# Optimization experiments

Measured on AMD Instinct MI355X. Metric: run time of the kernel, lower is better.

The kernel has to match this reference:

```python
import jax, jax.numpy as jnp
import numpy as np

N, C_IN, C_OUT, P, W, H = 32, 32, 16, 4, 16, 16
D = P * P
EPS = 1e-6


def squash(s, axis=-1):
    # v = ||s||^2/(1+||s||^2) * s/||s||, eps-stabilized as in the repo (eps=1e-6)
    n2 = jnp.sum(s * s, axis=axis, keepdims=True)
    n = jnp.sqrt(n2)
    return (n2 / (1.0 + n2)) * s / (n + EPS)


def setup_inputs() -> dict:
    key = jax.random.key(0)
    k1, k2, k3 = jax.random.split(key, 3)
    l = jax.random.normal(k1, (N, C_IN, D, W, H), jnp.float32)
    g = jax.random.normal(k2, (N, C_OUT, D), jnp.float32)
    weight = jax.random.normal(k3, (1, C_IN, 1, C_OUT, P, P), jnp.float32)
    return {"l": l, "g": g, "weight": weight, "num_iters": 3}


def reference(l, g, weight, num_iters):
    n, c, d, w, h = l.shape
    p = weight.shape[-1]
    c_out = weight.shape[3]
    # (N, C, D, W, H) -> (N, C, W*H, P, P)
    lp = jnp.transpose(l, (0, 1, 3, 4, 2)).reshape(n, c, w * h, p, p)
    # votes: pose matmul against per-(in,out) transform matrices
    # v[n,c,s,o] = lp[n,c,s] @ weight[0,c,0,o]   -> (N, C, WH, C_out, P, P)
    v = jnp.einsum('ncsij,cojk->ncsoik', lp, weight[0, :, 0])
    M = c * w * h
    v = v.reshape(n, M, c_out, d)          # (N, M, C_out, D)
    g = g[:, None, :, :]                    # (N, 1, C_out, D)
    # dynamic routing, logits initialized from agreement with the prior global capsule g
    b = jnp.sum(v * g, axis=-1, keepdims=True)   # (N, M, C_out, 1)
    cc = None
    for _ in range(num_iters):
        cc = jax.nn.softmax(b, axis=1)           # attention over input votes M
        g = squash(jnp.sum(cc * v, axis=1, keepdims=True))  # (N, 1, C_out, D)
        b = b + jnp.sum(v * g, axis=-1, keepdims=True)
    a = jnp.squeeze(cc, -1)   # (N, M, C_out)
    g = jnp.squeeze(g, 1)     # (N, C_out, D)
    return a, g
```

## Files before the change

kernel.cpp:

```cpp
#include <hip/hip_runtime.h>
#include <math.h>

#define N_   32
#define CIN  32
#define COUT 16
#define D_   16
#define S_   256
#define M_   (CIN * S_)

#define LOG2E 1.4426950408889634f

#define PROW 20
#define PIDX(n, c, o) ((((size_t)(n) * CIN + (c)) * COUT + (o)) * PROW)

#define WS_PB0 0
#define WS_PB1 (N_ * CIN * COUT * PROW)
#define WS_G1  (2 * N_ * CIN * COUT * PROW)

#define SW(s) ((((s) & 3)) ^ (((s) >> 2) & 3))

__device__ __forceinline__ void stage_tile(const float* __restrict__ gsrc,
                                           float* ls, int tid) {
  const float4* src = (const float4*)gsrc;
#pragma unroll
  for (int j = 0; j < 4; j++) {
    int f = ((tid & 3) << 6) + (tid >> 2) + (j << 8);
    float4 val = src[f];
    int dd = f >> 6;
    int u  = f & 63;
    int chunk = dd >> 2, lo = dd & 3;
    float vv[4] = {val.x, val.y, val.z, val.w};
#pragma unroll
    for (int m = 0; m < 4; m++) {
      int s = (u << 2) + m;
      int p = chunk ^ SW(s);
      ls[(s << 4) + (p << 2) + lo] = vv[m];
    }
  }
}

__device__ __forceinline__ void read_lp(const float* ls, int s, float* lp) {
  const float4* row = (const float4*)(ls + (s << 4));
  int sw = SW(s);
#pragma unroll
  for (int c = 0; c < 4; c++) {
    float4 q = row[c ^ sw];
    lp[c * 4 + 0] = q.x; lp[c * 4 + 1] = q.y;
    lp[c * 4 + 2] = q.z; lp[c * 4 + 3] = q.w;
  }
}

__device__ __forceinline__ float dot16(const float* a, const float* b) {
  float a0 = 0.f, a1 = 0.f, a2 = 0.f, a3 = 0.f;
#pragma unroll
  for (int k = 0; k < 4; k++) {
    a0 = fmaf(a[k],      b[k],      a0);
    a1 = fmaf(a[4 + k],  b[4 + k],  a1);
    a2 = fmaf(a[8 + k],  b[8 + k],  a2);
    a3 = fmaf(a[12 + k], b[12 + k], a3);
  }
  return (a0 + a1) + (a2 + a3);
}

__global__ __launch_bounds__(256, 3) void pass_kernel(
    const float* __restrict__ l, const float* __restrict__ wgt,
    const float* __restrict__ gprev, const float* __restrict__ part_in,
    float* __restrict__ gstore, float* __restrict__ part_out,
    float* __restrict__ edump, int mode) {
  const int bid = blockIdx.x;
  const int n = bid >> 5;
  const int c = bid & 31;
  const int tid = threadIdx.x;
  const int o = tid & 15;
  const int strip = tid >> 4;

  __shared__ float ls[D_ * S_];
  __shared__ float red[4][18][16];
  __shared__ float red2[18][16];
  __shared__ float hd[16][20];

  if (mode && tid < 64) {
    const int ho = tid & 15, hs = tid >> 4;
    float H[18];
#pragma unroll
    for (int f = 0; f < 17; f++) H[f] = 0.f;
    H[17] = -INFINITY;
#pragma unroll 2
    for (int q = 0; q < 8; q++) {
      const float* r = part_in + PIDX(n, hs + 4 * q, ho);
      const float4* r4 = (const float4*)r;
#pragma unroll
      for (int i = 0; i < 4; i++) {
        float4 v = r4[i];
        H[i * 4 + 0] += v.x; H[i * 4 + 1] += v.y;
        H[i * 4 + 2] += v.z; H[i * 4 + 3] += v.w;
      }
      H[16] += r[16];
      H[17] = fmaxf(H[17], r[17]);
    }
#pragma unroll
    for (int off = 16; off <= 32; off <<= 1) {
#pragma unroll
      for (int f = 0; f < 17; f++) H[f] += __shfl_xor(H[f], off);
      H[17] = fmaxf(H[17], __shfl_xor(H[17], off));
    }
    if (tid < 16) {
      float inv = 1.0f / H[16], n2 = 0.f, Sg[16];
#pragma unroll
      for (int d = 0; d < 16; d++) { Sg[d] = H[d] * inv; n2 = fmaf(Sg[d], Sg[d], n2); }
      float coef = n2 / ((1.f + n2) * (sqrtf(n2) + 1e-6f));
      float4* hq = (float4*)hd[tid];
#pragma unroll
      for (int i = 0; i < 4; i++)
        hq[i] = make_float4(coef * Sg[i * 4 + 0], coef * Sg[i * 4 + 1],
                            coef * Sg[i * 4 + 2], coef * Sg[i * 4 + 3]);
      hd[tid][16] = H[17];
    }
  }

  stage_tile(l + ((size_t)(n * CIN + c)) * D_ * S_, ls, tid);

  float Greg[16];
  {
    const float4* gp = (const float4*)(gprev + (n * COUT + o) * 16);
#pragma unroll
    for (int i = 0; i < 4; i++) {
      float4 u = gp[i];
      Greg[i * 4 + 0] = u.x; Greg[i * 4 + 1] = u.y;
      Greg[i * 4 + 2] = u.z; Greg[i * 4 + 3] = u.w;
    }
  }

  __syncthreads();

  float shift = 0.f;
  if (mode) {
    const float4* hq = (const float4*)hd[o];
#pragma unroll
    for (int i = 0; i < 4; i++) {
      float4 v = hq[i];
      Greg[i * 4 + 0] += v.x; Greg[i * 4 + 1] += v.y;
      Greg[i * 4 + 2] += v.z; Greg[i * 4 + 3] += v.w;
    }
    shift = hd[o][16];
    if (mode == 1 && c == 0 && tid < 16) {
      float* gs = gstore + (n * COUT + tid) * 16;
      const float4* hp = (const float4*)hd[tid];
      const float4* gp = (const float4*)(gprev + (n * COUT + tid) * 16);
      float4* g4 = (float4*)gs;
#pragma unroll
      for (int i = 0; i < 4; i++) {
        float4 a = gp[i], b = hp[i];
        g4[i] = make_float4(a.x + b.x, a.y + b.y, a.z + b.z, a.w + b.w);
      }
    }
  }

  float WG[16];
  {
    float wreg[16];
    const float4* wp = (const float4*)(wgt + (c * COUT + o) * 16);
#pragma unroll
    for (int i = 0; i < 4; i++) {
      float4 t = wp[i];
      wreg[i * 4 + 0] = t.x; wreg[i * 4 + 1] = t.y;
      wreg[i * 4 + 2] = t.z; wreg[i * 4 + 3] = t.w;
    }
#pragma unroll
    for (int i = 0; i < 4; i++)
#pragma unroll
      for (int j = 0; j < 4; j++) {
        float acc = 0.f;
#pragma unroll
        for (int k = 0; k < 4; k++)
          acc = fmaf(wreg[j * 4 + k], Greg[i * 4 + k], acc);
        WG[i * 4 + j] = acc * LOG2E;
      }
  }

  float se = 0.f, bmx = -INFINITY, E[16];
#pragma unroll
  for (int d = 0; d < 16; d++) E[d] = 0.f;

#pragma unroll 4
  for (int it = 0; it < 16; it++) {
    float lp[16];
    read_lp(ls, strip + (it << 4), lp);
    float b = dot16(lp, WG) - shift;
    float e = exp2f(b);
    if (mode == 2) {
      edump[((size_t)(n * M_ + c * S_ + strip + (it << 4))) * COUT + o] = e;
    }
    bmx = fmaxf(bmx, b);
    se += e;
#pragma unroll
    for (int d = 0; d < 16; d++) E[d] = fmaf(e, lp[d], E[d]);
  }

#pragma unroll
  for (int off = 16; off <= 32; off <<= 1) {
    se += __shfl_xor(se, off);
    bmx = fmaxf(bmx, __shfl_xor(bmx, off));
#pragma unroll
    for (int d = 0; d < 16; d++) E[d] += __shfl_xor(E[d], off);
  }

  const int w = tid >> 6;
  if ((tid & 63) < 16) {
#pragma unroll
    for (int d = 0; d < 16; d++) red[w][d][o] = E[d];
    red[w][16][o] = se;
    red[w][17][o] = bmx;
  }
  __syncthreads();

  for (int p = tid; p < 288; p += 256) {
    int f = p >> 4, oo = p & 15;
    float v0 = red[0][f][oo], v1 = red[1][f][oo];
    float v2 = red[2][f][oo], v3 = red[3][f][oo];
    red2[f][oo] = (f == 17) ? fmaxf(fmaxf(v0, v1), fmaxf(v2, v3))
                            : ((v0 + v1) + (v2 + v3));
  }
  __syncthreads();

  if (tid < 16) {
    float wt[16];
    const float4* wp = (const float4*)(wgt + (c * COUT + tid) * 16);
#pragma unroll
    for (int i = 0; i < 4; i++) {
      float4 t = wp[i];
      wt[i * 4 + 0] = t.x; wt[i * 4 + 1] = t.y;
      wt[i * 4 + 2] = t.z; wt[i * 4 + 3] = t.w;
    }
    float Et[16];
#pragma unroll
    for (int d = 0; d < 16; d++) Et[d] = red2[d][tid];
    float* p0 = part_out + PIDX(n, c, tid);
    float4* p4 = (float4*)p0;
#pragma unroll
    for (int i = 0; i < 4; i++) {
      float s0 = 0.f, s1 = 0.f, s2 = 0.f, s3 = 0.f;
#pragma unroll
      for (int j = 0; j < 4; j++) {
        s0 = fmaf(Et[i * 4 + j], wt[j * 4 + 0], s0);
        s1 = fmaf(Et[i * 4 + j], wt[j * 4 + 1], s1);
        s2 = fmaf(Et[i * 4 + j], wt[j * 4 + 2], s2);
        s3 = fmaf(Et[i * 4 + j], wt[j * 4 + 3], s3);
      }
      p4[i] = make_float4(s0, s1, s2, s3);
    }
    p0[16] = red2[16][tid];
    p0[17] = red2[17][tid] + shift;
  }
}

__global__ __launch_bounds__(256, 4) void a_kernel(
    const float* __restrict__ part, float* __restrict__ a_out,
    float* __restrict__ g_out) {
  const int bid = blockIdx.x;
  const int n = bid >> 6;
  const int chunk = bid & 63;
  const int tid = threadIdx.x;

  __shared__ float sinv[16];

  if (tid < 16) {
    float se = 0.f;
    if (chunk == 0) {
      float S[16];
#pragma unroll
      for (int d = 0; d < 16; d++) S[d] = 0.f;
#pragma unroll 4
      for (int c = 0; c < CIN; c++) {
        const float* r = part + PIDX(n, c, tid);
        const float4* r4 = (const float4*)r;
#pragma unroll
        for (int i = 0; i < 4; i++) {
          float4 v = r4[i];
          S[i * 4 + 0] += v.x; S[i * 4 + 1] += v.y;
          S[i * 4 + 2] += v.z; S[i * 4 + 3] += v.w;
        }
        se += r[16];
      }
      float inv = 1.0f / se, n2 = 0.f;
#pragma unroll
      for (int d = 0; d < 16; d++) { S[d] *= inv; n2 = fmaf(S[d], S[d], n2); }
      float coef = n2 / ((1.f + n2) * (sqrtf(n2) + 1e-6f));
      float* go = g_out + (n * COUT + tid) * 16;
#pragma unroll
      for (int d = 0; d < 16; d++) go[d] = coef * S[d];
      sinv[tid] = inv;
    } else {
#pragma unroll 8
      for (int c = 0; c < CIN; c++) se += part[PIDX(n, c, tid) + 16];
      sinv[tid] = 1.0f / se;
    }
  }
  __syncthreads();

  float4* pv = (float4*)(a_out + (size_t)n * (M_ * COUT) + (size_t)chunk * 2048);
#pragma unroll
  for (int r = 0; r < 2; r++) {
    int i4 = tid + (r << 8);
    int o0 = (i4 & 3) << 2;
    float4 v = pv[i4];
    v.x *= sinv[o0 + 0];
    v.y *= sinv[o0 + 1];
    v.z *= sinv[o0 + 2];
    v.w *= sinv[o0 + 3];
    pv[i4] = v;
  }
}

extern "C" void kernel_launch(void* const* d_in, const int* in_sizes, int n_in,
                              void* d_out, int out_size, void* d_ws, size_t ws_size,
                              hipStream_t stream) {
  const float* l = (const float*)d_in[0];
  const float* g = (const float*)d_in[1];
  const float* w = (const float*)d_in[2];

  float* out = (float*)d_out;
  float* ws = (float*)d_ws;
  float* a_out = out;
  float* g_out = out + (size_t)N_ * M_ * COUT;

  float* PB0 = ws + WS_PB0;
  float* PB1 = ws + WS_PB1;
  float* G1  = ws + WS_G1;

  pass_kernel<<<N_ * CIN, 256, 0, stream>>>(l, w, g, nullptr, nullptr, PB0,
                                            nullptr, 0);
  pass_kernel<<<N_ * CIN, 256, 0, stream>>>(l, w, g, PB0, G1, PB1,
                                            nullptr, 1);
  pass_kernel<<<N_ * CIN, 256, 0, stream>>>(l, w, G1, PB1, nullptr, PB0,
                                            a_out, 2);
  a_kernel<<<N_ * 64, 256, 0, stream>>>(PB0, a_out, g_out);
}
```

Before: 121.3 us.

## Fuse routing passes into one persistent kernel with grid barriers

Replaces the three pass launches and the final normalisation kernel with one kernel of 1024 blocks. Blocks synchronise between routing iterations through atomic-counter grid barriers, and the input tile stays resident in LDS across all passes instead of being restaged from global memory each time. The final pass writes the normalised attention directly, which removes the exp dump and the separate rescale read-modify-write over the large a output. This relies on all 1024 blocks being co-resident (4 per CU at the launch bound) and adds a memset launch plus barrier spin cost. The spin has a timeout, so if co-residency fails the barrier can break early and give wrong results instead of hanging.

New measurement: 411.4 us. +239.2%, slower.

```diff
diff --git a/kernel.cpp b/kernel.cpp
--- a/kernel.cpp
+++ b/kernel.cpp
@@ -7,15 +7,12 @@
 #define D_   16
 #define S_   256
 #define M_   (CIN * S_)
+#define NBLK (N_ * CIN)
 
 #define LOG2E 1.4426950408889634f
 
 #define PROW 20
 #define PIDX(n, c, o) ((((size_t)(n) * CIN + (c)) * COUT + (o)) * PROW)
-
-#define WS_PB0 0
-#define WS_PB1 (N_ * CIN * COUT * PROW)
-#define WS_G1  (2 * N_ * CIN * COUT * PROW)
 
 #define SW(s) ((((s) & 3)) ^ (((s) >> 2) & 3))
 
@@ -62,11 +59,184 @@
   return (a0 + a1) + (a2 + a3);
 }
 
-__global__ __launch_bounds__(256, 3) void pass_kernel(
+__device__ __forceinline__ void gbarrier(int* bar, int idx, int tid) {
+  __syncthreads();
+  if (tid == 0) {
+    __threadfence();
+    int* cnt = bar + 2 * idx;
+    int* flg = bar + 2 * idx + 1;
+    if (atomicAdd(cnt, 1) == NBLK - 1) {
+      __hip_atomic_store(flg, 1, __ATOMIC_RELEASE, __HIP_MEMORY_SCOPE_AGENT);
+    } else {
+      int guard = 0;
+      while (__hip_atomic_load(flg, __ATOMIC_ACQUIRE,
+                               __HIP_MEMORY_SCOPE_AGENT) == 0) {
+        __builtin_amdgcn_s_sleep(8);
+        if (++guard > 2000000) break;
+      }
+    }
+    __threadfence();
+  }
+  __syncthreads();
+}
+
+template <int PASS>
+__device__ __forceinline__ void routing_pass(
+    int n, int c, int tid, int o, int strip,
+    const float* __restrict__ wgt,
+    const float* __restrict__ part_in, float* __restrict__ part_out,
+    const float* ls, float red[4][18][16], float red2[18][16],
+    float hd[16][20], float* Gacc, float& shift) {
+  if constexpr (PASS > 0) {
+    if (tid < 64) {
+      const int ho = tid & 15, hs = tid >> 4;
+      float H[18];
+#pragma unroll
+      for (int f = 0; f < 17; f++) H[f] = 0.f;
+      H[17] = -INFINITY;
+#pragma unroll 2
+      for (int q = 0; q < 8; q++) {
+        const float* r = part_in + PIDX(n, hs + 4 * q, ho);
+        const float4* r4 = (const float4*)r;
+#pragma unroll
+        for (int i = 0; i < 4; i++) {
+          float4 v = r4[i];
+          H[i * 4 + 0] += v.x; H[i * 4 + 1] += v.y;
+          H[i * 4 + 2] += v.z; H[i * 4 + 3] += v.w;
+        }
+        H[16] += r[16];
+        H[17] = fmaxf(H[17], r[17]);
+      }
+#pragma unroll
+      for (int off = 16; off <= 32; off <<= 1) {
+#pragma unroll
+        for (int f = 0; f < 17; f++) H[f] += __shfl_xor(H[f], off);
+        H[17] = fmaxf(H[17], __shfl_xor(H[17], off));
+      }
+      if (tid < 16) {
+        float inv = 1.0f / H[16], n2 = 0.f, Sg[16];
+#pragma unroll
+        for (int d = 0; d < 16; d++) { Sg[d] = H[d] * inv; n2 = fmaf(Sg[d], Sg[d], n2); }
+        float coef = n2 / ((1.f + n2) * (sqrtf(n2) + 1e-6f));
+        float4* hq = (float4*)hd[tid];
+#pragma unroll
+        for (int i = 0; i < 4; i++)
+          hq[i] = make_float4(coef * Sg[i * 4 + 0], coef * Sg[i * 4 + 1],
+                              coef * Sg[i * 4 + 2], coef * Sg[i * 4 + 3]);
+        hd[tid][16] = H[17];
+      }
+    }
+    __syncthreads();
+    const float4* hq = (const float4*)hd[o];
+#pragma unroll
+    for (int i = 0; i < 4; i++) {
+      float4 v = hq[i];
+      Gacc[i * 4 + 0] += v.x; Gacc[i * 4 + 1] += v.y;
+      Gacc[i * 4 + 2] += v.z; Gacc[i * 4 + 3] += v.w;
+    }
+    shift = hd[o][16];
+  }
+
+  float WG[16];
+  {
+    float wreg[16];
+    const float4* wp = (const float4*)(wgt + (c * COUT + o) * 16);
+#pragma unroll
+    for (int i = 0; i < 4; i++) {
+      float4 t = wp[i];
+      wreg[i * 4 + 0] = t.x; wreg[i * 4 + 1] = t.y;
+      wreg[i * 4 + 2] = t.z; wreg[i * 4 + 3] = t.w;
+    }
+#pragma unroll
+    for (int i = 0; i < 4; i++)
+#pragma unroll
+      for (int j = 0; j < 4; j++) {
+        float acc = 0.f;
+#pragma unroll
+        for (int k = 0; k < 4; k++)
+          acc = fmaf(wreg[j * 4 + k], Gacc[i * 4 + k], acc);
+        WG[i * 4 + j] = acc * LOG2E;
+      }
+  }
+
+  float se = 0.f, bmx = -INFINITY, E[16];
+#pragma unroll
+  for (int d = 0; d < 16; d++) E[d] = 0.f;
+
+#pragma unroll 4
+  for (int it = 0; it < 16; it++) {
+    float lp[16];
+    read_lp(ls, strip + (it << 4), lp);
+    float b = dot16(lp, WG) - shift;
+    float e = exp2f(b);
+    bmx = fmaxf(bmx, b);
+    se += e;
+#pragma unroll
+    for (int d = 0; d < 16; d++) E[d] = fmaf(e, lp[d], E[d]);
+  }
+
+#pragma unroll
+  for (int off = 16; off <= 32; off <<= 1) {
+    se += __shfl_xor(se, off);
+    bmx = fmaxf(bmx, __shfl_xor(bmx, off));
+#pragma unroll
+    for (int d = 0; d < 16; d++) E[d] += __shfl_xor(E[d], off);
+  }
+
+  const int w = tid >> 6;
+  if ((tid & 63) < 16) {
+#pragma unroll
+    for (int d = 0; d < 16; d++) red[w][d][o] = E[d];
+    red[w][16][o] = se;
+    red[w][17][o] = bmx;
+  }
+  __syncthreads();
+
+  for (int p = tid; p < 288; p += 256) {
+    int f = p >> 4, oo = p & 15;
+    float v0 = red[0][f][oo], v1 = red[1][f][oo];
+    float v2 = red[2][f][oo], v3 = red[3][f][oo];
+    red2[f][oo] = (f == 17) ? fmaxf(fmaxf(v0, v1), fmaxf(v2, v3))
+                            : ((v0 + v1) + (v2 + v3));
+  }
+  __syncthreads();
+
+  if (tid < 16) {
+    float wt[16];
+    const float4* wp = (const float4*)(wgt + (c * COUT + tid) * 16);
+#pragma unroll
+    for (int i = 0; i < 4; i++) {
+      float4 t = wp[i];
+      wt[i * 4 + 0] = t.x; wt[i * 4 + 1] = t.y;
+      wt[i * 4 + 2] = t.z; wt[i * 4 + 3] = t.w;
+    }
+    float Et[16];
+#pragma unroll
+    for (int d = 0; d < 16; d++) Et[d] = red2[d][tid];
+    float* p0 = part_out + PIDX(n, c, tid);
+    float4* p4 = (float4*)p0;
+#pragma unroll
+    for (int i = 0; i < 4; i++) {
+      float s0 = 0.f, s1 = 0.f, s2 = 0.f, s3 = 0.f;
+#pragma unroll
+      for (int j = 0; j < 4; j++) {
+        s0 = fmaf(Et[i * 4 + j], wt[j * 4 + 0], s0);
+        s1 = fmaf(Et[i * 4 + j], wt[j * 4 + 1], s1);
+        s2 = fmaf(Et[i * 4 + j], wt[j * 4 + 2], s2);
+        s3 = fmaf(Et[i * 4 + j], wt[j * 4 + 3], s3);
+      }
+      p4[i] = make_float4(s0, s1, s2, s3);
+    }
+    p0[16] = red2[16][tid];
+    p0[17] = red2[17][tid] + shift;
+  }
+}
+
+__global__ __launch_bounds__(256, 4) void fused_kernel(
     const float* __restrict__ l, const float* __restrict__ wgt,
-    const float* __restrict__ gprev, const float* __restrict__ part_in,
-    float* __restrict__ gstore, float* __restrict__ part_out,
-    float* __restrict__ edump, int mode) {
+    const float* __restrict__ g0, float* __restrict__ a_out,
+    float* __restrict__ g_out, float* __restrict__ PB0,
+    float* __restrict__ PB1, int* __restrict__ bar) {
   const int bid = blockIdx.x;
   const int n = bid >> 5;
   const int c = bid & 31;
@@ -78,83 +248,68 @@
   __shared__ float red[4][18][16];
   __shared__ float red2[18][16];
   __shared__ float hd[16][20];
-
-  if (mode && tid < 64) {
-    const int ho = tid & 15, hs = tid >> 4;
-    float H[18];
-#pragma unroll
-    for (int f = 0; f < 17; f++) H[f] = 0.f;
-    H[17] = -INFINITY;
-#pragma unroll 2
-    for (int q = 0; q < 8; q++) {
-      const float* r = part_in + PIDX(n, hs + 4 * q, ho);
-      const float4* r4 = (const float4*)r;
-#pragma unroll
-      for (int i = 0; i < 4; i++) {
-        float4 v = r4[i];
-        H[i * 4 + 0] += v.x; H[i * 4 + 1] += v.y;
-        H[i * 4 + 2] += v.z; H[i * 4 + 3] += v.w;
-      }
-      H[16] += r[16];
-      H[17] = fmaxf(H[17], r[17]);
-    }
-#pragma unroll
-    for (int off = 16; off <= 32; off <<= 1) {
-#pragma unroll
-      for (int f = 0; f < 17; f++) H[f] += __shfl_xor(H[f], off);
-      H[17] = fmaxf(H[17], __shfl_xor(H[17], off));
-    }
-    if (tid < 16) {
-      float inv = 1.0f / H[16], n2 = 0.f, Sg[16];
-#pragma unroll
-      for (int d = 0; d < 16; d++) { Sg[d] = H[d] * inv; n2 = fmaf(Sg[d], Sg[d], n2); }
+  __shared__ float sinv[16];
+
+  stage_tile(l + ((size_t)(n * CIN + c)) * D_ * S_, ls, tid);
+
+  float Gacc[16];
+  {
+    const float4* gp = (const float4*)(g0 + (n * COUT + o) * 16);
+#pragma unroll
+    for (int i = 0; i < 4; i++) {
+      float4 u = gp[i];
+      Gacc[i * 4 + 0] = u.x; Gacc[i * 4 + 1] = u.y;
+      Gacc[i * 4 + 2] = u.z; Gacc[i * 4 + 3] = u.w;
+    }
+  }
+
+  __syncthreads();
+
+  float shift = 0.f;
+
+  routing_pass<0>(n, c, tid, o, strip, wgt, nullptr, PB0, ls, red, red2, hd,
+                  Gacc, shift);
+  gbarrier(bar, 0, tid);
+  routing_pass<1>(n, c, tid, o, strip, wgt, PB0, PB1, ls, red, red2, hd,
+                  Gacc, shift);
+  gbarrier(bar, 1, tid);
+  routing_pass<2>(n, c, tid, o, strip, wgt, PB1, PB0, ls, red, red2, hd,
+                  Gacc, shift);
+  gbarrier(bar, 2, tid);
+
+  if (tid < 16) {
+    float se = 0.f;
+    if (c == 0) {
+      float Ssum[16];
+#pragma unroll
+      for (int d = 0; d < 16; d++) Ssum[d] = 0.f;
+#pragma unroll 4
+      for (int cc = 0; cc < CIN; cc++) {
+        const float* r = PB0 + PIDX(n, cc, tid);
+        const float4* r4 = (const float4*)r;
+#pragma unroll
+        for (int i = 0; i < 4; i++) {
+          float4 v = r4[i];
+          Ssum[i * 4 + 0] += v.x; Ssum[i * 4 + 1] += v.y;
+          Ssum[i * 4 + 2] += v.z; Ssum[i * 4 + 3] += v.w;
+        }
+        se += r[16];
+      }
+      float inv = 1.0f / se, n2 = 0.f;
+#pragma unroll
+      for (int d = 0; d < 16; d++) { Ssum[d] *= inv; n2 = fmaf(Ssum[d], Ssum[d], n2); }
       float coef = n2 / ((1.f + n2) * (sqrtf(n2) + 1e-6f));
-      float4* hq = (float4*)hd[tid];
-#pragma unroll
-      for (int i = 0; i < 4; i++)
-        hq[i] = make_float4(coef * Sg[i * 4 + 0], coef * Sg[i * 4 + 1],
-                            coef * Sg[i * 4 + 2], coef * Sg[i * 4 + 3]);
-      hd[tid][16] = H[17];
-    }
-  }
-
-  stage_tile(l + ((size_t)(n * CIN + c)) * D_ * S_, ls, tid);
-
-  float Greg[16];
-  {
-    const float4* gp = (const float4*)(gprev + (n * COUT + o) * 16);
-#pragma unroll
-    for (int i = 0; i < 4; i++) {
-      float4 u = gp[i];
-      Greg[i * 4 + 0] = u.x; Greg[i * 4 + 1] = u.y;
-      Greg[i * 4 + 2] = u.z; Greg[i * 4 + 3] = u.w;
-    }
-  }
-
-  __syncthreads();
-
-  float shift = 0.f;
-  if (mode) {
-    const float4* hq = (const float4*)hd[o];
-#pragma unroll
-    for (int i = 0; i < 4; i++) {
-      float4 v = hq[i];
-      Greg[i * 4 + 0] += v.x; Greg[i * 4 + 1] += v.y;
-      Greg[i * 4 + 2] += v.z; Greg[i * 4 + 3] += v.w;
-    }
-    shift = hd[o][16];
-    if (mode == 1 && c == 0 && tid < 16) {
-      float* gs = gstore + (n * COUT + tid) * 16;
-      const float4* hp = (const float4*)hd[tid];
-      const float4* gp = (const float4*)(gprev + (n * COUT + tid) * 16);
-      float4* g4 = (float4*)gs;
-#pragma unroll
-      for (int i = 0; i < 4; i++) {
-        float4 a = gp[i], b = hp[i];
-        g4[i] = make_float4(a.x + b.x, a.y + b.y, a.z + b.z, a.w + b.w);
-      }
-    }
-  }
+      float* go = g_out + (n * COUT + tid) * 16;
+#pragma unroll
+      for (int d = 0; d < 16; d++) go[d] = coef * Ssum[d];
+      sinv[tid] = inv;
+    } else {
+#pragma unroll 8
+      for (int cc = 0; cc < CIN; cc++) se += PB0[PIDX(n, cc, tid) + 16];
+      sinv[tid] = 1.0f / se;
+    }
+  }
+  __syncthreads();
 
   float WG[16];
   {
@@ -173,142 +328,18 @@
         float acc = 0.f;
 #pragma unroll
         for (int k = 0; k < 4; k++)
-          acc = fmaf(wreg[j * 4 + k], Greg[i * 4 + k], acc);
+          acc = fmaf(wreg[j * 4 + k], Gacc[i * 4 + k], acc);
         WG[i * 4 + j] = acc * LOG2E;
       }
   }
-
-  float se = 0.f, bmx = -INFINITY, E[16];
-#pragma unroll
-  for (int d = 0; d < 16; d++) E[d] = 0.f;
-
+  const float myinv = sinv[o];
+  float* abase = a_out + ((size_t)(n * M_ + c * S_)) * COUT;
 #pragma unroll 4
   for (int it = 0; it < 16; it++) {
     float lp[16];
     read_lp(ls, strip + (it << 4), lp);
     float b = dot16(lp, WG) - shift;
-    float e = exp2f(b);
-    if (mode == 2) {
-      edump[((size_t)(n * M_ + c * S_ + strip + (it << 4))) * COUT + o] = e;
-    }
-    bmx = fmaxf(bmx, b);
-    se += e;
-#pragma unroll
-    for (int d = 0; d < 16; d++) E[d] = fmaf(e, lp[d], E[d]);
-  }
-
-#pragma unroll
-  for (int off = 16; off <= 32; off <<= 1) {
-    se += __shfl_xor(se, off);
-    bmx = fmaxf(bmx, __shfl_xor(bmx, off));
-#pragma unroll
-    for (int d = 0; d < 16; d++) E[d] += __shfl_xor(E[d], off);
-  }
-
-  const int w = tid >> 6;
-  if ((tid & 63) < 16) {
-#pragma unroll
-    for (int d = 0; d < 16; d++) red[w][d][o] = E[d];
-    red[w][16][o] = se;
-    red[w][17][o] = bmx;
-  }
-  __syncthreads();
-
-  for (int p = tid; p < 288; p += 256) {
-    int f = p >> 4, oo = p & 15;
-    float v0 = red[0][f][oo], v1 = red[1][f][oo];
-    float v2 = red[2][f][oo], v3 = red[3][f][oo];
-    red2[f][oo] = (f == 17) ? fmaxf(fmaxf(v0, v1), fmaxf(v2, v3))
-                            : ((v0 + v1) + (v2 + v3));
-  }
-  __syncthreads();
-
-  if (tid < 16) {
-    float wt[16];
-    const float4* wp = (const float4*)(wgt + (c * COUT + tid) * 16);
-#pragma unroll
-    for (int i = 0; i < 4; i++) {
-      float4 t = wp[i];
-      wt[i * 4 + 0] = t.x; wt[i * 4 + 1] = t.y;
-      wt[i * 4 + 2] = t.z; wt[i * 4 + 3] = t.w;
-    }
-    float Et[16];
-#pragma unroll
-    for (int d = 0; d < 16; d++) Et[d] = red2[d][tid];
-    float* p0 = part_out + PIDX(n, c, tid);
-    float4* p4 = (float4*)p0;
-#pragma unroll
-    for (int i = 0; i < 4; i++) {
-      float s0 = 0.f, s1 = 0.f, s2 = 0.f, s3 = 0.f;
-#pragma unroll
-      for (int j = 0; j < 4; j++) {
-        s0 = fmaf(Et[i * 4 + j], wt[j * 4 + 0], s0);
-        s1 = fmaf(Et[i * 4 + j], wt[j * 4 + 1], s1);
-        s2 = fmaf(Et[i * 4 + j], wt[j * 4 + 2], s2);
-        s3 = fmaf(Et[i * 4 + j], wt[j * 4 + 3], s3);
-      }
-      p4[i] = make_float4(s0, s1, s2, s3);
-    }
-    p0[16] = red2[16][tid];
-    p0[17] = red2[17][tid] + shift;
-  }
-}
-
-__global__ __launch_bounds__(256, 4) void a_kernel(
-    const float* __restrict__ part, float* __restrict__ a_out,
-    float* __restrict__ g_out) {
-  const int bid = blockIdx.x;
-  const int n = bid >> 6;
-  const int chunk = bid & 63;
-  const int tid = threadIdx.x;
-
-  __shared__ float sinv[16];
-
-  if (tid < 16) {
-    float se = 0.f;
-    if (chunk == 0) {
-      float S[16];
-#pragma unroll
-      for (int d = 0; d < 16; d++) S[d] = 0.f;
-#pragma unroll 4
-      for (int c = 0; c < CIN; c++) {
-        const float* r = part + PIDX(n, c, tid);
-        const float4* r4 = (const float4*)r;
-#pragma unroll
-        for (int i = 0; i < 4; i++) {
-          float4 v = r4[i];
-          S[i * 4 + 0] += v.x; S[i * 4 + 1] += v.y;
-          S[i * 4 + 2] += v.z; S[i * 4 + 3] += v.w;
-        }
-        se += r[16];
-      }
-      float inv = 1.0f / se, n2 = 0.f;
-#pragma unroll
-      for (int d = 0; d < 16; d++) { S[d] *= inv; n2 = fmaf(S[d], S[d], n2); }
-      float coef = n2 / ((1.f + n2) * (sqrtf(n2) + 1e-6f));
-      float* go = g_out + (n * COUT + tid) * 16;
-#pragma unroll
-      for (int d = 0; d < 16; d++) go[d] = coef * S[d];
-      sinv[tid] = inv;
-    } else {
-#pragma unroll 8
-      for (int c = 0; c < CIN; c++) se += part[PIDX(n, c, tid) + 16];
-      sinv[tid] = 1.0f / se;
-    }
-  }
-  __syncthreads();
-
-  float4* pv = (float4*)(a_out + (size_t)n * (M_ * COUT) + (size_t)chunk * 2048);
-#pragma unroll
-  for (int r = 0; r < 2; r++) {
-    int i4 = tid + (r << 8);
-    int o0 = (i4 & 3) << 2;
-    float4 v = pv[i4];
-    v.x *= sinv[o0 + 0];
-    v.y *= sinv[o0 + 1];
-    v.z *= sinv[o0 + 2];
-    v.w *= sinv[o0 + 3];
-    pv[i4] = v;
+    abase[(size_t)((strip + (it << 4)) * COUT + o)] = exp2f(b) * myinv;
   }
 }
 
@@ -320,19 +351,15 @@
   const float* w = (const float*)d_in[2];
 
   float* out = (float*)d_out;
-  float* ws = (float*)d_ws;
   float* a_out = out;
   float* g_out = out + (size_t)N_ * M_ * COUT;
 
-  float* PB0 = ws + WS_PB0;
-  float* PB1 = ws + WS_PB1;
-  float* G1  = ws + WS_G1;
-
-  pass_kernel<<<N_ * CIN, 256, 0, stream>>>(l, w, g, nullptr, nullptr, PB0,
-                                            nullptr, 0);
-  pass_kernel<<<N_ * CIN, 256, 0, stream>>>(l, w, g, PB0, G1, PB1,
-                                            nullptr, 1);
-  pass_kernel<<<N_ * CIN, 256, 0, stream>>>(l, w, G1, PB1, nullptr, PB0,
-                                            a_out, 2);
-  a_kernel<<<N_ * 64, 256, 0, stream>>>(PB0, a_out, g_out);
-}
+  float* ws = (float*)d_ws;
+  float* PB0 = ws;
+  float* PB1 = ws + (size_t)N_ * CIN * COUT * PROW;
+  int* bar = (int*)(ws + 2 * (size_t)N_ * CIN * COUT * PROW);
+
+  hipMemsetAsync(bar, 0, 8 * sizeof(int), stream);
+
+  fused_kernel<<<NBLK, 256, 0, stream>>>(l, w, g, a_out, g_out, PB0, PB1, bar);
+}
```
